# Performance work log

Measured on AMD Instinct MI355X. Metric: run time of the kernel, lower is better.

## Reference

```python
import jax, jax.numpy as jnp
import numpy as np

N, K, D = 65536, 1024, 256


def setup_inputs() -> dict:
    key = jax.random.key(0)
    k1, k2 = jax.random.split(key)
    input_data = jax.random.normal(k1, (N, D), dtype=jnp.float32)
    codebooks = jax.random.normal(k2, (K, D), dtype=jnp.float32)
    return {"input_data": input_data, "codebooks": codebooks}


def reference(input_data, codebooks):
    # Squared Euclidean distances [N, K] via the expanded form
    # in the torch source, without the [N, D, K] intermediate).
    x_sq = jnp.sum(input_data * input_data, axis=-1, keepdims=True)      # [N, 1]
    c_sq = jnp.sum(codebooks * codebooks, axis=-1)                       # [K]
    distances = x_sq + c_sq[None, :] - 2.0 * (input_data @ codebooks.T)  # [N, K]

    min_indices = jnp.argmin(distances, axis=1)                          # [N]
    quantized_input = codebooks[min_indices]                             # [N, D]

    loss = jnp.mean(jnp.square(input_data - quantized_input))

    # avg_probs = mean over rows of one_hot(min_indices, K) == counts / N
    counts = jnp.zeros((K,), dtype=jnp.float32).at[min_indices].add(1.0)
    avg_probs = counts / jnp.float32(N)
    perplexity = jnp.exp(-jnp.sum(avg_probs * jnp.log(avg_probs + 1e-10)))

    return quantized_input, loss, perplexity, min_indices
```

## Files before the change

### kernel.cpp

```cpp
#include <hip/hip_runtime.h>
#include <math.h>

#define N_ROWS 65536
#define K_CODES 1024
#define D_DIM 256
#define TAU 0.12f

#define WS_NFLAG   0
#define WS_CSQ     16
#define WS_COUNTS  4112
#define WS_MINIDX  8208
#define WS_LIST    270352
#define WS_PART    532496
#define WS_CSQD    534544
#define WS_CBH     542736

typedef _Float16 f16x8 __attribute__((ext_vector_type(8)));
typedef float    f32x4 __attribute__((ext_vector_type(4)));

__device__ __forceinline__ void gl_lds16(const _Float16* g, _Float16* l) {
    __builtin_amdgcn_global_load_lds(
        (const __attribute__((address_space(1))) unsigned int*)g,
        (__attribute__((address_space(3))) unsigned int*)l, 16, 0, 0);
}

__global__ __launch_bounds__(256) void k_prep(
    const float* __restrict__ x, const float* __restrict__ cb,
    _Float16* __restrict__ xh, _Float16* __restrict__ cbh,
    float* __restrict__ xsq, float* __restrict__ csq, double* __restrict__ csqd,
    float* __restrict__ cbT, unsigned* __restrict__ counts, unsigned* __restrict__ nflag)
{
    const int b = blockIdx.x;
    const int t = threadIdx.x;
    if (b < 8192) {
        const long idx8 = (long)b * 2048 + t * 8;
        float4 v0 = *(const float4*)(x + idx8);
        float4 v1 = *(const float4*)(x + idx8 + 4);
        f16x8 h;
        h[0] = (_Float16)v0.x; h[1] = (_Float16)v0.y; h[2] = (_Float16)v0.z; h[3] = (_Float16)v0.w;
        h[4] = (_Float16)v1.x; h[5] = (_Float16)v1.y; h[6] = (_Float16)v1.z; h[7] = (_Float16)v1.w;
        *(f16x8*)(xh + idx8) = h;
        float sq = v0.x * v0.x + v0.y * v0.y + v0.z * v0.z + v0.w * v0.w
                 + v1.x * v1.x + v1.y * v1.y + v1.z * v1.z + v1.w * v1.w;
        for (int off = 16; off > 0; off >>= 1) sq += __shfl_down(sq, off, 32);
        if ((t & 31) == 0) xsq[b * 8 + (t >> 5)] = sq;
    } else {
        const int b2 = b - 8192;
        const long idx8 = (long)b2 * 2048 + t * 8;
        float4 v0 = *(const float4*)(cb + idx8);
        float4 v1 = *(const float4*)(cb + idx8 + 4);
        f16x8 h;
        h[0] = (_Float16)v0.x; h[1] = (_Float16)v0.y; h[2] = (_Float16)v0.z; h[3] = (_Float16)v0.w;
        h[4] = (_Float16)v1.x; h[5] = (_Float16)v1.y; h[6] = (_Float16)v1.z; h[7] = (_Float16)v1.w;
        *(f16x8*)(cbh + idx8) = h;
        {
            const int row = b2 * 8 + (t >> 5);
            const int col = (t & 31) * 8;
            cbT[(col + 0) * 1024 + row] = v0.x;
            cbT[(col + 1) * 1024 + row] = v0.y;
            cbT[(col + 2) * 1024 + row] = v0.z;
            cbT[(col + 3) * 1024 + row] = v0.w;
            cbT[(col + 4) * 1024 + row] = v1.x;
            cbT[(col + 5) * 1024 + row] = v1.y;
            cbT[(col + 6) * 1024 + row] = v1.z;
            cbT[(col + 7) * 1024 + row] = v1.w;
        }
        double sqd = (double)v0.x * v0.x + (double)v0.y * v0.y
                   + (double)v0.z * v0.z + (double)v0.w * v0.w
                   + (double)v1.x * v1.x + (double)v1.y * v1.y
                   + (double)v1.z * v1.z + (double)v1.w * v1.w;
        for (int off = 16; off > 0; off >>= 1) sqd += __shfl_down(sqd, off, 32);
        if ((t & 31) == 0) {
            csqd[b2 * 8 + (t >> 5)] = sqd;
            csq[b2 * 8 + (t >> 5)] = (float)sqd;
        }
        if (b2 < 4) counts[b2 * 256 + t] = 0u;
        if (b2 == 0 && t == 0) *nflag = 0u;
    }
}

__device__ __forceinline__ void merge2(float& m1, int& i1, float& m2,
                                       float om1, int oi1, float om2) {
    float hi  = fmaxf(m1, om1);
    float lo2 = fminf(m2, om2);
    bool take = (om1 < m1) || (om1 == m1 && oi1 < i1);
    if (take) { m1 = om1; i1 = oi1; }
    m2 = fminf(hi, lo2);
}

__global__ __launch_bounds__(256) void k_main(
    const _Float16* __restrict__ xh, const _Float16* __restrict__ cbh,
    const float* __restrict__ csq,
    float* __restrict__ m1h, float* __restrict__ m2h, float* __restrict__ i1f)
{
    __shared__ __attribute__((aligned(16))) _Float16 As[128 * 32];
    __shared__ __attribute__((aligned(16))) _Float16 Bs[128 * 32];

    const int tid  = threadIdx.x;
    const int w    = tid >> 6;
    const int lane = tid & 63;
    const int rlow = lane & 15;
    const int quad = lane >> 4;
    const int rowTile = blockIdx.x >> 1;
    const int half    = blockIdx.x & 1;
    const long n0  = (long)rowTile * 128;
    const int khalf = half * 512;

    float sm1[8], sm2[8];
    int   si1[8];
#pragma unroll
    for (int s = 0; s < 8; s++) { sm1[s] = INFINITY; sm2[s] = INFINITY; si1[s] = 0; }

    for (int kt = 0; kt < 4; ++kt) {
        const int kbase = khalf + kt * 128;
        f32x4 acc[16];
        const f32x4 z = {0.f, 0.f, 0.f, 0.f};
#pragma unroll
        for (int t = 0; t < 16; t++) acc[t] = z;

        for (int d0 = 0; d0 < 256; d0 += 32) {
            __syncthreads();
#pragma unroll
            for (int r = 0; r < 2; ++r) {
                int o = r * 256 + tid;
                gl_lds16(xh  + (n0 + (o >> 2)) * 256 + d0 + (o & 3) * 8, As + o * 8);
                gl_lds16(cbh + (long)(kbase + (o >> 2)) * 256 + d0 + (o & 3) * 8, Bs + o * 8);
            }
            __syncthreads();

            f16x8 a[2], b[8];
#pragma unroll
            for (int i = 0; i < 2; ++i)
                a[i] = *(const f16x8*)&As[(w * 32 + i * 16 + rlow) * 32 + quad * 8];
#pragma unroll
            for (int j = 0; j < 8; ++j)
                b[j] = *(const f16x8*)&Bs[(j * 16 + rlow) * 32 + quad * 8];
#pragma unroll
            for (int i = 0; i < 2; ++i)
#pragma unroll
                for (int j = 0; j < 8; ++j)
                    acc[i * 8 + j] = __builtin_amdgcn_mfma_f32_16x16x32_f16(
                        a[i], b[j], acc[i * 8 + j], 0, 0, 0);
        }

#pragma unroll
        for (int j = 0; j < 8; ++j) {
            const int code = kbase + j * 16 + rlow;
            const float csj = csq[code];
#pragma unroll
            for (int i = 0; i < 2; ++i)
#pragma unroll
                for (int v = 0; v < 4; ++v) {
                    const int s = i * 4 + v;
                    float val = fmaf(-2.f, acc[i * 8 + j][v], csj);
                    bool lt = val < sm1[s];
                    sm2[s] = fminf(fmaxf(val, sm1[s]), sm2[s]);
                    si1[s] = lt ? code : si1[s];
                    sm1[s] = fminf(val, sm1[s]);
                }
        }
    }

#pragma unroll
    for (int s = 0; s < 8; ++s) {
#pragma unroll
        for (int m = 1; m < 16; m <<= 1) {
            float om1 = __shfl_xor(sm1[s], m, 64);
            float om2 = __shfl_xor(sm2[s], m, 64);
            int   oi1 = __shfl_xor(si1[s], m, 64);
            merge2(sm1[s], si1[s], sm2[s], om1, oi1, om2);
        }
    }

    if (rlow == 0) {
        const long hb = (long)half * 65536;
#pragma unroll
        for (int i = 0; i < 2; ++i)
#pragma unroll
            for (int v = 0; v < 4; ++v) {
                const int s = i * 4 + v;
                long n = n0 + w * 32 + i * 16 + quad * 4 + v;
                m1h[hb + n] = sm1[s];
                m2h[hb + n] = sm2[s];
                i1f[hb + n] = (float)si1[s];
            }
    }
}

__global__ __launch_bounds__(256) void k_merge(
    const float* __restrict__ m1h, const float* __restrict__ m2h,
    const float* __restrict__ i1f, const float* __restrict__ xsq,
    int* __restrict__ min_idx, int* __restrict__ list,
    unsigned* __restrict__ nflag, double* __restrict__ partials)
{
    __shared__ double red[256];
    const int tid = threadIdx.x;
    const int n = blockIdx.x * 256 + tid;

    float m1a = m1h[n], m1b = m1h[65536 + n];
    float m2a = m2h[n], m2b = m2h[65536 + n];
    int   ia  = (int)i1f[n], ib = (int)i1f[65536 + n];

    bool bw = (m1b < m1a) || (m1b == m1a && ib < ia);
    float m1 = bw ? m1b : m1a;
    int   i1 = bw ? ib : ia;
    float m2 = fminf(bw ? m1a : m1b, bw ? m2b : m2a);

    min_idx[n] = i1;
    if (m2 - m1 < TAU) { unsigned p = atomicAdd(nflag, 1u); list[p] = n; }

    red[tid] = (double)xsq[n] + (double)m1;
    __syncthreads();
    for (int off = 128; off > 0; off >>= 1) {
        if (tid < off) red[tid] += red[tid + off];
        __syncthreads();
    }
    if (tid == 0) partials[blockIdx.x] = red[0];
}

#define RPB 2
__global__ __launch_bounds__(256) void k_refine(
    const float* __restrict__ x, const float* __restrict__ cbT,
    const double* __restrict__ csqd, const unsigned* __restrict__ nflag,
    const int* __restrict__ list, int* __restrict__ min_idx)
{
    __shared__ double xsd[RPB][256];
    __shared__ double rbv[RPB][4];
    __shared__ int    rbi[RPB][4];
    const int tid = threadIdx.x;
    const int w = tid >> 6, lane = tid & 63;
    const unsigned nf = *nflag;
    const int k0 = tid * 4;

    for (unsigned base = blockIdx.x * RPB; base < nf; base += gridDim.x * RPB) {
        __syncthreads();
#pragma unroll
        for (int r = 0; r < RPB; ++r) {
            unsigned it = base + r; if (it > nf - 1) it = nf - 1;
            int ridx = list[it];
            xsd[r][tid] = (double)x[(long)ridx * D_DIM + tid];
        }
        __syncthreads();

        double s0[RPB], s1[RPB], s2[RPB], s3[RPB];
#pragma unroll
        for (int r = 0; r < RPB; ++r) { s0[r] = 0.0; s1[r] = 0.0; s2[r] = 0.0; s3[r] = 0.0; }

#pragma unroll 4
        for (int d = 0; d < D_DIM; ++d) {
            float4 c = *(const float4*)(cbT + d * 1024 + k0);
            double c0 = (double)c.x, c1 = (double)c.y;
            double c2 = (double)c.z, c3 = (double)c.w;
#pragma unroll
            for (int r = 0; r < RPB; ++r) {
                double xv = xsd[r][d];
                s0[r] = fma(xv, c0, s0[r]);
                s1[r] = fma(xv, c1, s1[r]);
                s2[r] = fma(xv, c2, s2[r]);
                s3[r] = fma(xv, c3, s3[r]);
            }
        }

        double best[RPB]; int bidx[RPB];
#pragma unroll
        for (int r = 0; r < RPB; ++r) { best[r] = 1e300; bidx[r] = 0; }
        {
            const double ck0 = csqd[k0];
            const double ck1 = csqd[k0 + 1];
            const double ck2 = csqd[k0 + 2];
            const double ck3 = csqd[k0 + 3];
#pragma unroll
            for (int r = 0; r < RPB; ++r) {
                double dd;
                dd = fma(-2.0, s0[r], ck0);
                if (dd < best[r] || (dd == best[r] && k0 < bidx[r])) { best[r] = dd; bidx[r] = k0; }
                dd = fma(-2.0, s1[r], ck1);
                if (dd < best[r] || (dd == best[r] && k0 + 1 < bidx[r])) { best[r] = dd; bidx[r] = k0 + 1; }
                dd = fma(-2.0, s2[r], ck2);
                if (dd < best[r] || (dd == best[r] && k0 + 2 < bidx[r])) { best[r] = dd; bidx[r] = k0 + 2; }
                dd = fma(-2.0, s3[r], ck3);
                if (dd < best[r] || (dd == best[r] && k0 + 3 < bidx[r])) { best[r] = dd; bidx[r] = k0 + 3; }
            }
        }

#pragma unroll
        for (int r = 0; r < RPB; ++r) {
            double bv = best[r]; int bi = bidx[r];
            for (int off = 32; off > 0; off >>= 1) {
                double od = __shfl_down(bv, off, 64);
                int    oi = __shfl_down(bi, off, 64);
                if (od < bv || (od == bv && oi < bi)) { bv = od; bi = oi; }
            }
            if (lane == 0) { rbv[r][w] = bv; rbi[r][w] = bi; }
        }
        __syncthreads();
        if (tid < RPB && base + tid < nf) {
            double bb = rbv[tid][0]; int bi_ = rbi[tid][0];
#pragma unroll
            for (int wv = 1; wv < 4; ++wv) {
                if (rbv[tid][wv] < bb || (rbv[tid][wv] == bb && rbi[tid][wv] < bi_)) {
                    bb = rbv[tid][wv]; bi_ = rbi[tid][wv];
                }
            }
            min_idx[list[base + tid]] = bi_;
        }
    }
}

__global__ __launch_bounds__(256) void k_out(
    const float* __restrict__ cb, const int* __restrict__ min_idx,
    float* __restrict__ out, unsigned* __restrict__ counts)
{
    const int tid  = threadIdx.x;
    const int wave = tid >> 6;
    const int lane = tid & 63;
    const long n = (long)blockIdx.x * 4 + wave;
    const int idx = min_idx[n];

    float4 q = *(const float4*)(cb + (long)idx * D_DIM + lane * 4);
    *(float4*)(out + n * D_DIM + lane * 4) = q;

    if (lane == 0) {
        atomicAdd(&counts[idx], 1u);
        out[16777218L + n] = (float)idx;
    }
}

__global__ void k_final(const double* __restrict__ partials,
                        const unsigned* __restrict__ counts, float* __restrict__ out)
{
    __shared__ double red[256];
    const int tid = threadIdx.x;

    red[tid] = partials[tid];
    __syncthreads();
    for (int off = 128; off > 0; off >>= 1) { if (tid < off) red[tid] += red[tid + off]; __syncthreads(); }
    double loss = red[0] / (double)((long)N_ROWS * D_DIM);
    __syncthreads();

    double h = 0.0;
    for (int k = tid; k < K_CODES; k += 256) {
        double p = (double)counts[k] / (double)N_ROWS;
        h += p * log(p + 1e-10);
    }
    red[tid] = h;
    __syncthreads();
    for (int off = 128; off > 0; off >>= 1) { if (tid < off) red[tid] += red[tid + off]; __syncthreads(); }

    if (tid == 0) {
        out[16777216] = (float)loss;
        out[16777217] = (float)exp(-red[0]);
    }
}

extern "C" void kernel_launch(void* const* d_in, const int* in_sizes, int n_in,
                              void* d_out, int out_size, void* d_ws, size_t ws_size,
                              hipStream_t stream)
{
    const float* x  = (const float*)d_in[0];
    const float* cb = (const float*)d_in[1];
    float* out = (float*)d_out;
    char*  ws  = (char*)d_ws;

    unsigned*  nflag    = (unsigned*)(ws + WS_NFLAG);
    float*     csq      = (float*)(ws + WS_CSQ);
    unsigned*  counts   = (unsigned*)(ws + WS_COUNTS);
    int*       min_idx  = (int*)(ws + WS_MINIDX);
    int*       list     = (int*)(ws + WS_LIST);
    double*    partials = (double*)(ws + WS_PART);
    double*    csqd     = (double*)(ws + WS_CSQD);
    _Float16*  cbh      = (_Float16*)(ws + WS_CBH);
    _Float16*  xh       = (_Float16*)d_out;
    float*     m1h      = out + 8388608L;
    float*     m2h      = out + 8519680L;
    float*     i1f      = out + 8650752L;
    float*     cbT      = out + 8781824L;
    float*     xsq      = out + 16777218L;

    hipLaunchKernelGGL(k_prep,   dim3(8192 + 128), dim3(256), 0, stream,
                       x, cb, xh, cbh, xsq, csq, csqd, cbT, counts, nflag);
    hipLaunchKernelGGL(k_main,   dim3(1024), dim3(256), 0, stream,
                       xh, cbh, csq, m1h, m2h, i1f);
    hipLaunchKernelGGL(k_merge,  dim3(256), dim3(256), 0, stream,
                       m1h, m2h, i1f, xsq, min_idx, list, nflag, partials);
    hipLaunchKernelGGL(k_refine, dim3(1024), dim3(256), 0, stream,
                       x, cbT, csqd, nflag, list, min_idx);
    hipLaunchKernelGGL(k_out,    dim3(N_ROWS / 4), dim3(256), 0, stream,
                       cb, min_idx, out, counts);
    hipLaunchKernelGGL(k_final,  dim3(1), dim3(256), 0, stream, partials, counts, out);
}
```

Baseline: 263.6 us.

## Fuse x fp16 conversion and merge into main GEMM with register-resident A tiles

The main kernel now loads x directly in fp32, converts it to fp16 into registers for the whole D dimension, and computes row norms inline. This removes the xh prep pass and the separate merge kernel. Each block covers all 1024 codes instead of half, and codebook tiles are double-buffered in swizzled LDS with 64-wide D chunks. Min-index selection, refine-list append and loss partials move into the main kernel's epilogue. In exchange, register pressure rises from keeping A in registers, and the grid shrinks to 512 blocks, which may limit occupancy and parallelism.

```diff
diff --git a/kernel.cpp b/kernel.cpp
--- a/kernel.cpp
+++ b/kernel.cpp
@@ -12,8 +12,8 @@
 #define WS_MINIDX  8208
 #define WS_LIST    270352
 #define WS_PART    532496
-#define WS_CSQD    534544
-#define WS_CBH     542736
+#define WS_CSQD    536592
+#define WS_CBH     544784
 
 typedef _Float16 f16x8 __attribute__((ext_vector_type(8)));
 typedef float    f32x4 __attribute__((ext_vector_type(4)));
@@ -25,58 +25,43 @@
 }
 
 __global__ __launch_bounds__(256) void k_prep(
-    const float* __restrict__ x, const float* __restrict__ cb,
-    _Float16* __restrict__ xh, _Float16* __restrict__ cbh,
-    float* __restrict__ xsq, float* __restrict__ csq, double* __restrict__ csqd,
-    float* __restrict__ cbT, unsigned* __restrict__ counts, unsigned* __restrict__ nflag)
-{
-    const int b = blockIdx.x;
+    const float* __restrict__ cb, _Float16* __restrict__ cbh,
+    float* __restrict__ csq, double* __restrict__ csqd,
+    float* __restrict__ cbT, unsigned* __restrict__ counts,
+    unsigned* __restrict__ nflag)
+{
+    const int b2 = blockIdx.x;
     const int t = threadIdx.x;
-    if (b < 8192) {
-        const long idx8 = (long)b * 2048 + t * 8;
-        float4 v0 = *(const float4*)(x + idx8);
-        float4 v1 = *(const float4*)(x + idx8 + 4);
-        f16x8 h;
-        h[0] = (_Float16)v0.x; h[1] = (_Float16)v0.y; h[2] = (_Float16)v0.z; h[3] = (_Float16)v0.w;
-        h[4] = (_Float16)v1.x; h[5] = (_Float16)v1.y; h[6] = (_Float16)v1.z; h[7] = (_Float16)v1.w;
-        *(f16x8*)(xh + idx8) = h;
-        float sq = v0.x * v0.x + v0.y * v0.y + v0.z * v0.z + v0.w * v0.w
-                 + v1.x * v1.x + v1.y * v1.y + v1.z * v1.z + v1.w * v1.w;
-        for (int off = 16; off > 0; off >>= 1) sq += __shfl_down(sq, off, 32);
-        if ((t & 31) == 0) xsq[b * 8 + (t >> 5)] = sq;
-    } else {
-        const int b2 = b - 8192;
-        const long idx8 = (long)b2 * 2048 + t * 8;
-        float4 v0 = *(const float4*)(cb + idx8);
-        float4 v1 = *(const float4*)(cb + idx8 + 4);
-        f16x8 h;
-        h[0] = (_Float16)v0.x; h[1] = (_Float16)v0.y; h[2] = (_Float16)v0.z; h[3] = (_Float16)v0.w;
-        h[4] = (_Float16)v1.x; h[5] = (_Float16)v1.y; h[6] = (_Float16)v1.z; h[7] = (_Float16)v1.w;
-        *(f16x8*)(cbh + idx8) = h;
-        {
-            const int row = b2 * 8 + (t >> 5);
-            const int col = (t & 31) * 8;
-            cbT[(col + 0) * 1024 + row] = v0.x;
-            cbT[(col + 1) * 1024 + row] = v0.y;
-            cbT[(col + 2) * 1024 + row] = v0.z;
-            cbT[(col + 3) * 1024 + row] = v0.w;
-            cbT[(col + 4) * 1024 + row] = v1.x;
-            cbT[(col + 5) * 1024 + row] = v1.y;
-            cbT[(col + 6) * 1024 + row] = v1.z;
-            cbT[(col + 7) * 1024 + row] = v1.w;
-        }
-        double sqd = (double)v0.x * v0.x + (double)v0.y * v0.y
-                   + (double)v0.z * v0.z + (double)v0.w * v0.w
-                   + (double)v1.x * v1.x + (double)v1.y * v1.y
-                   + (double)v1.z * v1.z + (double)v1.w * v1.w;
-        for (int off = 16; off > 0; off >>= 1) sqd += __shfl_down(sqd, off, 32);
-        if ((t & 31) == 0) {
-            csqd[b2 * 8 + (t >> 5)] = sqd;
-            csq[b2 * 8 + (t >> 5)] = (float)sqd;
-        }
-        if (b2 < 4) counts[b2 * 256 + t] = 0u;
-        if (b2 == 0 && t == 0) *nflag = 0u;
-    }
+    const long idx8 = (long)b2 * 2048 + t * 8;
+    float4 v0 = *(const float4*)(cb + idx8);
+    float4 v1 = *(const float4*)(cb + idx8 + 4);
+    f16x8 h;
+    h[0] = (_Float16)v0.x; h[1] = (_Float16)v0.y; h[2] = (_Float16)v0.z; h[3] = (_Float16)v0.w;
+    h[4] = (_Float16)v1.x; h[5] = (_Float16)v1.y; h[6] = (_Float16)v1.z; h[7] = (_Float16)v1.w;
+    *(f16x8*)(cbh + idx8) = h;
+    {
+        const int row = b2 * 8 + (t >> 5);
+        const int col = (t & 31) * 8;
+        cbT[(col + 0) * 1024 + row] = v0.x;
+        cbT[(col + 1) * 1024 + row] = v0.y;
+        cbT[(col + 2) * 1024 + row] = v0.z;
+        cbT[(col + 3) * 1024 + row] = v0.w;
+        cbT[(col + 4) * 1024 + row] = v1.x;
+        cbT[(col + 5) * 1024 + row] = v1.y;
+        cbT[(col + 6) * 1024 + row] = v1.z;
+        cbT[(col + 7) * 1024 + row] = v1.w;
+    }
+    double sqd = (double)v0.x * v0.x + (double)v0.y * v0.y
+               + (double)v0.z * v0.z + (double)v0.w * v0.w
+               + (double)v1.x * v1.x + (double)v1.y * v1.y
+               + (double)v1.z * v1.z + (double)v1.w * v1.w;
+    for (int off = 16; off > 0; off >>= 1) sqd += __shfl_down(sqd, off, 32);
+    if ((t & 31) == 0) {
+        csqd[b2 * 8 + (t >> 5)] = sqd;
+        csq[b2 * 8 + (t >> 5)] = (float)sqd;
+    }
+    if (b2 < 4) counts[b2 * 256 + t] = 0u;
+    if (b2 == 0 && t == 0) *nflag = 0u;
 }
 
 __device__ __forceinline__ void merge2(float& m1, int& i1, float& m2,
@@ -88,77 +73,123 @@
     m2 = fminf(hi, lo2);
 }
 
-__global__ __launch_bounds__(256) void k_main(
-    const _Float16* __restrict__ xh, const _Float16* __restrict__ cbh,
+__global__ __launch_bounds__(256, 2) void k_main(
+    const float* __restrict__ x, const _Float16* __restrict__ cbh,
     const float* __restrict__ csq,
-    float* __restrict__ m1h, float* __restrict__ m2h, float* __restrict__ i1f)
-{
-    __shared__ __attribute__((aligned(16))) _Float16 As[128 * 32];
-    __shared__ __attribute__((aligned(16))) _Float16 Bs[128 * 32];
+    int* __restrict__ min_idx, int* __restrict__ list,
+    unsigned* __restrict__ nflag, double* __restrict__ partials)
+{
+    __shared__ __attribute__((aligned(16))) _Float16 Bs[2][128 * 64];
+    __shared__ float  xsq_s[128];
+    __shared__ double wred[4];
 
     const int tid  = threadIdx.x;
     const int w    = tid >> 6;
     const int lane = tid & 63;
     const int rlow = lane & 15;
     const int quad = lane >> 4;
-    const int rowTile = blockIdx.x >> 1;
-    const int half    = blockIdx.x & 1;
-    const long n0  = (long)rowTile * 128;
-    const int khalf = half * 512;
+    const long n0  = (long)blockIdx.x * 128;
+
+#pragma unroll
+    for (int r = 0; r < 4; ++r) {
+        int o = r * 256 + tid;
+        int row = o >> 3, s = o & 7, g = s ^ (row & 7);
+        gl_lds16(cbh + (long)row * 256 + g * 8, Bs[0] + o * 8);
+    }
+
+    f16x8 a_reg[8][2];
+#pragma unroll
+    for (int i = 0; i < 2; ++i) {
+        float cs[8];
+        const float* rp = x + (n0 + w * 32 + i * 16 + rlow) * 256;
+#pragma unroll
+        for (int c = 0; c < 8; ++c) {
+            const float* src = rp + c * 32 + quad * 8;
+            float4 v0 = *(const float4*)src;
+            float4 v1 = *(const float4*)(src + 4);
+            f16x8 h;
+            h[0] = (_Float16)v0.x; h[1] = (_Float16)v0.y; h[2] = (_Float16)v0.z; h[3] = (_Float16)v0.w;
+            h[4] = (_Float16)v1.x; h[5] = (_Float16)v1.y; h[6] = (_Float16)v1.z; h[7] = (_Float16)v1.w;
+            a_reg[c][i] = h;
+            cs[c] = v0.x * v0.x + v0.y * v0.y + v0.z * v0.z + v0.w * v0.w
+                  + v1.x * v1.x + v1.y * v1.y + v1.z * v1.z + v1.w * v1.w;
+        }
+        float s1_0 = cs[0] + cs[4], s1_1 = cs[1] + cs[5];
+        float s1_2 = cs[2] + cs[6], s1_3 = cs[3] + cs[7];
+        float s2_0 = s1_0 + s1_2, s2_1 = s1_1 + s1_3;
+        float s3 = s2_0 + s2_1;
+        float s4 = s3 + __shfl_down(s3, 32, 64);
+        float s5 = s4 + __shfl_down(s4, 16, 64);
+        if (quad == 0) xsq_s[w * 32 + i * 16 + rlow] = s5;
+    }
 
     float sm1[8], sm2[8];
     int   si1[8];
 #pragma unroll
     for (int s = 0; s < 8; s++) { sm1[s] = INFINITY; sm2[s] = INFINITY; si1[s] = 0; }
 
-    for (int kt = 0; kt < 4; ++kt) {
-        const int kbase = khalf + kt * 128;
-        f32x4 acc[16];
-        const f32x4 z = {0.f, 0.f, 0.f, 0.f};
-#pragma unroll
-        for (int t = 0; t < 16; t++) acc[t] = z;
-
-        for (int d0 = 0; d0 < 256; d0 += 32) {
-            __syncthreads();
-#pragma unroll
-            for (int r = 0; r < 2; ++r) {
+    f32x4 acc[16];
+    const f32x4 z = {0.f, 0.f, 0.f, 0.f};
+#pragma unroll
+    for (int t2 = 0; t2 < 16; t2++) acc[t2] = z;
+
+    __syncthreads();
+
+    for (int p = 0; p < 32; ++p) {
+        const int cur = p & 1;
+        if (p < 31) {
+            const int pn = p + 1;
+            const long kb = (long)(pn >> 2) * 128;
+            const int d0 = (pn & 3) * 64;
+            _Float16* dst = Bs[cur ^ 1];
+#pragma unroll
+            for (int r = 0; r < 4; ++r) {
                 int o = r * 256 + tid;
-                gl_lds16(xh  + (n0 + (o >> 2)) * 256 + d0 + (o & 3) * 8, As + o * 8);
-                gl_lds16(cbh + (long)(kbase + (o >> 2)) * 256 + d0 + (o & 3) * 8, Bs + o * 8);
-            }
-            __syncthreads();
-
-            f16x8 a[2], b[8];
-#pragma unroll
-            for (int i = 0; i < 2; ++i)
-                a[i] = *(const f16x8*)&As[(w * 32 + i * 16 + rlow) * 32 + quad * 8];
-#pragma unroll
-            for (int j = 0; j < 8; ++j)
-                b[j] = *(const f16x8*)&Bs[(j * 16 + rlow) * 32 + quad * 8];
+                int row = o >> 3, s = o & 7, g = s ^ (row & 7);
+                gl_lds16(cbh + (kb + row) * 256 + d0 + g * 8, dst + o * 8);
+            }
+        }
+        const int kt = p >> 2, dblk = p & 3;
+        const _Float16* B = Bs[cur];
+#pragma unroll
+        for (int h = 0; h < 2; ++h) {
+            f16x8 b[8];
+#pragma unroll
+            for (int j = 0; j < 8; ++j) {
+                int row = j * 16 + rlow;
+                int s = (h * 4 + quad) ^ (rlow & 7);
+                b[j] = *(const f16x8*)&B[row * 64 + s * 8];
+            }
+            const int c = dblk * 2 + h;
 #pragma unroll
             for (int i = 0; i < 2; ++i)
 #pragma unroll
                 for (int j = 0; j < 8; ++j)
                     acc[i * 8 + j] = __builtin_amdgcn_mfma_f32_16x16x32_f16(
-                        a[i], b[j], acc[i * 8 + j], 0, 0, 0);
-        }
-
-#pragma unroll
-        for (int j = 0; j < 8; ++j) {
-            const int code = kbase + j * 16 + rlow;
-            const float csj = csq[code];
-#pragma unroll
-            for (int i = 0; i < 2; ++i)
-#pragma unroll
-                for (int v = 0; v < 4; ++v) {
-                    const int s = i * 4 + v;
-                    float val = fmaf(-2.f, acc[i * 8 + j][v], csj);
-                    bool lt = val < sm1[s];
-                    sm2[s] = fminf(fmaxf(val, sm1[s]), sm2[s]);
-                    si1[s] = lt ? code : si1[s];
-                    sm1[s] = fminf(val, sm1[s]);
-                }
-        }
+                        a_reg[c][i], b[j], acc[i * 8 + j], 0, 0, 0);
+        }
+        if (dblk == 3) {
+            const int kbase = kt * 128;
+#pragma unroll
+            for (int j = 0; j < 8; ++j) {
+                const int code = kbase + j * 16 + rlow;
+                const float csj = csq[code];
+#pragma unroll
+                for (int i = 0; i < 2; ++i)
+#pragma unroll
+                    for (int v = 0; v < 4; ++v) {
+                        const int s = i * 4 + v;
+                        float val = fmaf(-2.f, acc[i * 8 + j][v], csj);
+                        bool lt = val < sm1[s];
+                        sm2[s] = fminf(fmaxf(val, sm1[s]), sm2[s]);
+                        si1[s] = lt ? code : si1[s];
+                        sm1[s] = fminf(val, sm1[s]);
+                    }
+            }
+#pragma unroll
+            for (int t2 = 0; t2 < 16; ++t2) acc[t2] = z;
+        }
+        __syncthreads();
     }
 
 #pragma unroll
@@ -172,50 +203,28 @@
         }
     }
 
+    double lsum = 0.0;
     if (rlow == 0) {
-        const long hb = (long)half * 65536;
 #pragma unroll
         for (int i = 0; i < 2; ++i)
 #pragma unroll
             for (int v = 0; v < 4; ++v) {
                 const int s = i * 4 + v;
-                long n = n0 + w * 32 + i * 16 + quad * 4 + v;
-                m1h[hb + n] = sm1[s];
-                m2h[hb + n] = sm2[s];
-                i1f[hb + n] = (float)si1[s];
-            }
-    }
-}
-
-__global__ __launch_bounds__(256) void k_merge(
-    const float* __restrict__ m1h, const float* __restrict__ m2h,
-    const float* __restrict__ i1f, const float* __restrict__ xsq,
-    int* __restrict__ min_idx, int* __restrict__ list,
-    unsigned* __restrict__ nflag, double* __restrict__ partials)
-{
-    __shared__ double red[256];
-    const int tid = threadIdx.x;
-    const int n = blockIdx.x * 256 + tid;
-
-    float m1a = m1h[n], m1b = m1h[65536 + n];
-    float m2a = m2h[n], m2b = m2h[65536 + n];
-    int   ia  = (int)i1f[n], ib = (int)i1f[65536 + n];
-
-    bool bw = (m1b < m1a) || (m1b == m1a && ib < ia);
-    float m1 = bw ? m1b : m1a;
-    int   i1 = bw ? ib : ia;
-    float m2 = fminf(bw ? m1a : m1b, bw ? m2b : m2a);
-
-    min_idx[n] = i1;
-    if (m2 - m1 < TAU) { unsigned p = atomicAdd(nflag, 1u); list[p] = n; }
-
-    red[tid] = (double)xsq[n] + (double)m1;
-    __syncthreads();
-    for (int off = 128; off > 0; off >>= 1) {
-        if (tid < off) red[tid] += red[tid + off];
-        __syncthreads();
-    }
-    if (tid == 0) partials[blockIdx.x] = red[0];
+                const int rl = w * 32 + i * 16 + quad * 4 + v;
+                const long n = n0 + rl;
+                min_idx[n] = si1[s];
+                if (sm2[s] - sm1[s] < TAU) {
+                    unsigned pp = atomicAdd(nflag, 1u);
+                    list[pp] = (int)n;
+                }
+                lsum += (double)xsq_s[rl] + (double)sm1[s];
+            }
+    }
+    lsum += __shfl_down(lsum, 32, 64);
+    lsum += __shfl_down(lsum, 16, 64);
+    if (lane == 0) wred[w] = lsum;
+    __syncthreads();
+    if (tid == 0) partials[blockIdx.x] = ((wred[0] + wred[1]) + wred[2]) + wred[3];
 }
 
 #define RPB 2
@@ -332,7 +341,7 @@
     __shared__ double red[256];
     const int tid = threadIdx.x;
 
-    red[tid] = partials[tid];
+    red[tid] = partials[tid] + partials[tid + 256];
     __syncthreads();
     for (int off = 128; off > 0; off >>= 1) { if (tid < off) red[tid] += red[tid + off]; __syncthreads(); }
     double loss = red[0] / (double)((long)N_ROWS * D_DIM);
@@ -370,19 +379,12 @@
     double*    partials = (double*)(ws + WS_PART);
     double*    csqd     = (double*)(ws + WS_CSQD);
     _Float16*  cbh      = (_Float16*)(ws + WS_CBH);
-    _Float16*  xh       = (_Float16*)d_out;
-    float*     m1h      = out + 8388608L;
-    float*     m2h      = out + 8519680L;
-    float*     i1f      = out + 8650752L;
     float*     cbT      = out + 8781824L;
-    float*     xsq      = out + 16777218L;
-
-    hipLaunchKernelGGL(k_prep,   dim3(8192 + 128), dim3(256), 0, stream,
-                       x, cb, xh, cbh, xsq, csq, csqd, cbT, counts, nflag);
-    hipLaunchKernelGGL(k_main,   dim3(1024), dim3(256), 0, stream,
-                       xh, cbh, csq, m1h, m2h, i1f);
-    hipLaunchKernelGGL(k_merge,  dim3(256), dim3(256), 0, stream,
-                       m1h, m2h, i1f, xsq, min_idx, list, nflag, partials);
+
+    hipLaunchKernelGGL(k_prep,   dim3(128),  dim3(256), 0, stream,
+                       cb, cbh, csq, csqd, cbT, counts, nflag);
+    hipLaunchKernelGGL(k_main,   dim3(512),  dim3(256), 0, stream,
+                       x, cbh, csq, min_idx, list, nflag, partials);
     hipLaunchKernelGGL(k_refine, dim3(1024), dim3(256), 0, stream,
                        x, cbT, csqd, nflag, list, min_idx);
     hipLaunchKernelGGL(k_out,    dim3(N_ROWS / 4), dim3(256), 0, stream,
```

Result: no change. 262.9 us (-0.3%).
